# Kernel tuning notes

Hardware: AMD Instinct MI355X
Metric: run time of the kernel (lower is better)

## Reference

```python
import jax, jax.numpy as jnp
import numpy as np

N = 25000      # nodes
E = 400000     # edges
D = 128        # num_hidden (per-head out dim)
H = 3          # heads
NEG_SLOPE = 0.2
BN_EPS = 1e-5


def _gatv2(x, edge_index, Wl, bl, Wr, br, att, bias):
    """PyG GATv2Conv (concat=True, add_self_loops=True, dropout=0).
    x: [N, Din]; Wl/Wr: [Din, H*D]; att: [H, D]; bias: [H*D].
    """
    n = x.shape[0]
    h, d = att.shape
    loops = jnp.arange(n)
    src = jnp.concatenate([edge_index[0], loops])  # [E+N]
    dst = jnp.concatenate([edge_index[1], loops])
    xl = (x @ Wl + bl).reshape(n, h, d)  # source transform
    xr = (x @ Wr + br).reshape(n, h, d)  # target transform
    # edge scores: a^T LeakyReLU(xl_j + xr_i)
    e = jax.nn.leaky_relu(xl[src] + xr[dst], NEG_SLOPE)   # [E+N, H, D]
    score = jnp.einsum('ehd,hd->eh', e, att)              # [E+N, H]
    # segment softmax over incoming edges of each dst node
    m = jax.ops.segment_max(score, dst, num_segments=n)   # [N, H]
    ex = jnp.exp(score - m[dst])
    denom = jax.ops.segment_sum(ex, dst, num_segments=n)  # [N, H]
    alpha = ex / denom[dst]                               # [E+N, H]
    out = jax.ops.segment_sum(alpha[:, :, None] * xl[src], dst, num_segments=n)
    return out.reshape(n, h * d) + bias                   # [N, H*D]


def _batchnorm(x, gamma, beta):
    mu = jnp.mean(x, axis=0)
    var = jnp.var(x, axis=0)  # biased, as torch BN uses for normalization
    return gamma * (x - mu) * jax.lax.rsqrt(var + BN_EPS) + beta


def setup_inputs() -> dict:
    key = jax.random.key(0)
    ks = iter(jax.random.split(key, 32))
    s = 0.1
    p = {}
    p['x'] = jax.random.normal(next(ks), (N, D), jnp.float32)
    p['edge_index'] = jax.random.randint(next(ks), (2, E), 0, N, jnp.int64)
    for i in (1, 2):
        p[f'Wl{i}'] = s * jax.random.normal(next(ks), (D, H * D), jnp.float32)
        p[f'bl{i}'] = jnp.zeros((H * D,), jnp.float32)
        p[f'Wr{i}'] = s * jax.random.normal(next(ks), (D, H * D), jnp.float32)
        p[f'br{i}'] = jnp.zeros((H * D,), jnp.float32)
        p[f'att{i}'] = s * jax.random.normal(next(ks), (H, D), jnp.float32)
        p[f'bc{i}'] = jnp.zeros((H * D,), jnp.float32)
        p[f'g{i}'] = jnp.ones((D,), jnp.float32)
        p[f'be{i}'] = jnp.zeros((D,), jnp.float32)
    p['W1'] = s * jax.random.normal(next(ks), (H * D, D), jnp.float32)
    p['b1'] = jnp.zeros((D,), jnp.float32)
    p['W2'] = s * jax.random.normal(next(ks), (2 * H * D, D), jnp.float32)
    p['b2'] = jnp.zeros((D,), jnp.float32)
    return p


def reference(x, edge_index, Wl1, bl1, Wr1, br1, att1, bc1, g1, be1,
              Wl2, bl2, Wr2, br2, att2, bc2, g2, be2, W1, b1, W2, b2):
    x_in = _gatv2(x, edge_index, Wl1, bl1, Wr1, br1, att1, bc1)  # [N, H*D]
    h = _batchnorm(x_in @ W1 + b1, g1, be1)
    h = jax.nn.relu(h)                                           # [N, D]
    h2 = _gatv2(h, edge_index, Wl2, bl2, Wr2, br2, att2, bc2)    # [N, H*D]
    out = jnp.concatenate([h2, x_in], axis=1) @ W2 + b2          # [N, D]
    out = _batchnorm(out, g2, be2)
    return jax.nn.relu(out)
```

## Files before the change

### kernel.cpp

```cpp
#include <hip/hip_runtime.h>
#include <math.h>

#define NN 25000
#define NE 400000
#define DD 128
#define HD 384
#define NEG 0.2f
#define EPS 1e-5f

typedef unsigned int u32;
typedef unsigned short u16;
typedef __attribute__((ext_vector_type(8))) short short8;
typedef __attribute__((ext_vector_type(4))) float floatx4;

__device__ __forceinline__ u32 bf16_1(float x) {
    u32 u = __float_as_uint(x);
    return (u + 0x7fffu + ((u >> 16) & 1u)) >> 16;
}
__device__ __forceinline__ float blo(u32 u) { return __uint_as_float(u << 16); }
__device__ __forceinline__ float bhi(u32 u) { return __uint_as_float(u & 0xffff0000u); }

__device__ __forceinline__ void up8(uint4 u, float* f) {
    f[0] = blo(u.x); f[1] = bhi(u.x); f[2] = blo(u.y); f[3] = bhi(u.y);
    f[4] = blo(u.z); f[5] = bhi(u.z); f[6] = blo(u.w); f[7] = bhi(u.w);
}


__global__ void k_scan1(const int* __restrict__ cnt, int* __restrict__ bsum) {
    __shared__ int sh[256];
    int i = blockIdx.x * 256 + threadIdx.x;
    sh[threadIdx.x] = (i < NN) ? (cnt[i] + 1) : 0;
    __syncthreads();
    for (int o = 128; o >= 1; o >>= 1) {
        if ((int)threadIdx.x < o) sh[threadIdx.x] += sh[threadIdx.x + o];
        __syncthreads();
    }
    if (threadIdx.x == 0) bsum[blockIdx.x] = sh[0];
}

__global__ void k_scan3(const int* __restrict__ cnt, const int* __restrict__ bsum,
                        int* __restrict__ row_ptr, int* __restrict__ col_src,
                        int* __restrict__ cur) {
    __shared__ int sh[256];
    __shared__ int sb[128];
    int tid = threadIdx.x;
    if (tid < 128) sb[tid] = (tid < 98) ? bsum[tid] : 0;
    __syncthreads();
    for (int o = 1; o < 128; o <<= 1) {
        int t = (tid >= o && tid < 128) ? sb[tid - o] : 0;
        __syncthreads();
        if (tid < 128) sb[tid] += t;
        __syncthreads();
    }
    int i = blockIdx.x * 256 + tid;
    int v = (i < NN) ? (cnt[i] + 1) : 0;
    sh[tid] = v;
    __syncthreads();
    for (int o = 1; o < 256; o <<= 1) {
        int t = (tid >= o) ? sh[tid - o] : 0;
        __syncthreads();
        sh[tid] += t;
        __syncthreads();
    }
    int base = blockIdx.x ? sb[blockIdx.x - 1] : 0;
    if (i < NN) {
        int incl = base + sh[tid];
        row_ptr[i + 1] = incl;
        int p = incl - v;
        col_src[p] = i;
        cur[i] = p + 1;
    }
    if (i == 0) row_ptr[0] = 0;
}

__global__ void k_fill_edges(const int* __restrict__ src, const int* __restrict__ dst,
                             int* __restrict__ cur, int* __restrict__ col_src) {
    int e = blockIdx.x * 256 + threadIdx.x;
    if (e < NE) { int p = atomicAdd(&cur[dst[e]], 1); col_src[p] = src[e]; }
}

__global__ void k_cast_all(const float* __restrict__ x,
                           const float* __restrict__ Wl1, const float* __restrict__ Wr1,
                           const float* __restrict__ W1,
                           const float* __restrict__ Wl2, const float* __restrict__ Wr2,
                           const float* __restrict__ W2,
                           const float* __restrict__ bl1, const float* __restrict__ br1,
                           const float* __restrict__ bl2, const float* __restrict__ br2,
                           const int* __restrict__ edst,
                           u16* __restrict__ xb, u16* __restrict__ WfT1,
                           u16* __restrict__ W1T, u16* __restrict__ WfT2,
                           u16* __restrict__ W2T,
                           float* __restrict__ fb1, float* __restrict__ fb2,
                           int* __restrict__ cnt, float* __restrict__ stats) {
    int i = blockIdx.x * 256 + threadIdx.x;
    if (i < 400000) {
        const float4* xp = (const float4*)(x + (size_t)i * 8);
        float4 a = xp[0], b = xp[1];
        uint4 w;
        w.x = bf16_1(a.x) | (bf16_1(a.y) << 16);
        w.y = bf16_1(a.z) | (bf16_1(a.w) << 16);
        w.z = bf16_1(b.x) | (bf16_1(b.y) << 16);
        w.w = bf16_1(b.z) | (bf16_1(b.w) << 16);
        *(uint4*)(xb + (size_t)i * 8) = w;
        return;
    }
    i -= 400000;
    if (i < 400000) { atomicAdd(&cnt[edst[i]], 1); return; }
    i -= 400000;
    if (i < 49152) { int k = i / 384, n = i - k * 384; WfT1[n * 128 + k] = (u16)bf16_1(Wl1[i]); return; }
    i -= 49152;
    if (i < 49152) { int k = i / 384, n = i - k * 384; WfT1[(384 + n) * 128 + k] = (u16)bf16_1(Wr1[i]); return; }
    i -= 49152;
    if (i < 49152) { int k = i / 128, n = i - k * 128; W1T[n * 384 + k] = (u16)bf16_1(W1[i]); return; }
    i -= 49152;
    if (i < 49152) { int k = i / 384, n = i - k * 384; WfT2[n * 128 + k] = (u16)bf16_1(Wl2[i]); return; }
    i -= 49152;
    if (i < 49152) { int k = i / 384, n = i - k * 384; WfT2[(384 + n) * 128 + k] = (u16)bf16_1(Wr2[i]); return; }
    i -= 49152;
    if (i < 98304) { int k = i / 128, n = i - k * 128; W2T[n * 768 + k] = (u16)bf16_1(W2[i]); return; }
    i -= 98304;
    if (i < 768) { fb1[i] = (i < 384) ? bl1[i] : br1[i - 384]; return; }
    i -= 768;
    if (i < 768) { fb2[i] = (i < 384) ? bl2[i] : br2[i - 384]; return; }
    i -= 768;
    if (i < 512) stats[i] = 0.f;
}
#define CAST_TOTAL (400000 + 400000 + 5 * 49152 + 98304 + 1536 + 512)

__global__ __launch_bounds__(256) void k_gemm_k128(
        const u16* __restrict__ A, const u16* __restrict__ BT,
        const float* __restrict__ bias, u16* __restrict__ Cb, int M) {
    __shared__ short sA[128 * 128];
    __shared__ short sB[128 * 128];
    int tid = threadIdx.x;
    int wv = tid >> 6, lane = tid & 63;
    int quad = lane >> 4, m16 = lane & 15;
    int mb = blockIdx.y * 128, nb = blockIdx.x * 128;

#pragma unroll
    for (int j = 0; j < 8; ++j) {
        int L = j * 256 + tid;
        int r = L >> 4, c8 = (L & 15) ^ (r & 15);
        int gr = mb + r; gr = gr < M ? gr : M - 1;
        __builtin_amdgcn_global_load_lds(
            (const __attribute__((address_space(1))) void*)(A + (size_t)gr * 128 + c8 * 8),
            (__attribute__((address_space(3))) void*)(sA + (size_t)L * 8), 16, 0, 0);
    }
#pragma unroll
    for (int j = 0; j < 8; ++j) {
        int L = j * 256 + tid;
        int r = L >> 4, c8 = (L & 15) ^ (r & 15);
        __builtin_amdgcn_global_load_lds(
            (const __attribute__((address_space(1))) void*)(BT + (size_t)(nb + r) * 128 + c8 * 8),
            (__attribute__((address_space(3))) void*)(sB + (size_t)L * 8), 16, 0, 0);
    }
    __syncthreads();

    floatx4 acc[2][8];
#pragma unroll
    for (int mf = 0; mf < 2; ++mf)
#pragma unroll
        for (int nf = 0; nf < 8; ++nf)
#pragma unroll
            for (int r = 0; r < 4; ++r) acc[mf][nf][r] = 0.f;

#pragma unroll
    for (int ks = 0; ks < 4; ++ks) {
        int slot = (ks * 4 + quad) ^ m16;
        int row0 = wv * 32 + m16, row1 = row0 + 16;
        short8 a0 = *(const short8*)(sA + ((size_t)row0 * 16 + slot) * 8);
        short8 a1 = *(const short8*)(sA + ((size_t)row1 * 16 + slot) * 8);
#pragma unroll
        for (int nf = 0; nf < 8; ++nf) {
            short8 b = *(const short8*)(sB + ((size_t)(nf * 16 + m16) * 16 + slot) * 8);
            acc[0][nf] = __builtin_amdgcn_mfma_f32_16x16x32_bf16(a0, b, acc[0][nf], 0, 0, 0);
            acc[1][nf] = __builtin_amdgcn_mfma_f32_16x16x32_bf16(a1, b, acc[1][nf], 0, 0, 0);
        }
    }
    __syncthreads();

#pragma unroll
    for (int mf = 0; mf < 2; ++mf)
#pragma unroll
        for (int nf = 0; nf < 8; ++nf)
#pragma unroll
            for (int r = 0; r < 4; ++r) {
                int row = wv * 32 + mf * 16 + quad * 4 + r;
                int col = nf * 16 + m16;
                sA[row * 128 + col] = (short)bf16_1(acc[mf][nf][r] + bias[nb + col]);
            }
    __syncthreads();
    int xr = nb >= 384;
    int h = (xr ? (nb - 384) : nb) >> 7;
    u16* cb = Cb + ((size_t)(xr * 3 + h) * NN) * 128;
#pragma unroll
    for (int i = 0; i < 8; ++i) {
        int u = i * 256 + tid;
        int row = u >> 4, c8 = u & 15;
        int grow = mb + row;
        if (grow < M)
            *(uint4*)(cb + (size_t)grow * 128 + c8 * 8) = *(const uint4*)(sA + (size_t)u * 8);
    }
}

__global__ __launch_bounds__(256) void k_gemm_bf(
        const u16* __restrict__ A, const u16* __restrict__ BT,
        const float* __restrict__ bias,
        float* __restrict__ Cf, float* __restrict__ stats,
        int M, int N, int K, int lda) {
    __shared__ short smem[9216];
    short* sA = smem;
    short* sB = smem + 4096;
    int tid = threadIdx.x;
    int wv = tid >> 6, lane = tid & 63;
    int quad = lane >> 4, m16 = lane & 15;
    int sw = m16 & 7;
    int mb = blockIdx.y * 64, nb = blockIdx.x * 64;

    floatx4 acc[4];
#pragma unroll
    for (int nf = 0; nf < 4; ++nf)
#pragma unroll
        for (int r = 0; r < 4; ++r) acc[nf][r] = 0.f;

    for (int k0 = 0; k0 < K; k0 += 64) {
#pragma unroll
        for (int j = 0; j < 2; ++j) {
            int L = j * 256 + tid;
            int r = L >> 3, c8 = (L & 7) ^ (r & 7);
            int gr = mb + r; gr = gr < M ? gr : M - 1;
            __builtin_amdgcn_global_load_lds(
                (const __attribute__((address_space(1))) void*)(A + (size_t)gr * lda + k0 + c8 * 8),
                (__attribute__((address_space(3))) void*)(sA + (size_t)L * 8), 16, 0, 0);
        }
#pragma unroll
        for (int j = 0; j < 2; ++j) {
            int L = j * 256 + tid;
            int r = L >> 3, c8 = (L & 7) ^ (r & 7);
            __builtin_amdgcn_global_load_lds(
                (const __attribute__((address_space(1))) void*)(BT + (size_t)(nb + r) * K + k0 + c8 * 8),
                (__attribute__((address_space(3))) void*)(sB + (size_t)L * 8), 16, 0, 0);
        }
        __syncthreads();
#pragma unroll
        for (int ks = 0; ks < 2; ++ks) {
            int t = (ks * 4 + quad) ^ sw;
            const short* pa = sA + t * 8;
            const short* pb = sB + t * 8;
            short8 a0 = *(const short8*)(pa + (wv * 16 + m16) * 64);
#pragma unroll
            for (int nf = 0; nf < 4; ++nf) {
                short8 b = *(const short8*)(pb + (nf * 16 + m16) * 64);
                acc[nf] = __builtin_amdgcn_mfma_f32_16x16x32_bf16(a0, b, acc[nf], 0, 0, 0);
            }
        }
        __syncthreads();
    }
    float* fs = (float*)smem;
#pragma unroll
    for (int nf = 0; nf < 4; ++nf)
#pragma unroll
        for (int r = 0; r < 4; ++r) {
            int row = wv * 16 + quad * 4 + r;
            int col = nf * 16 + m16;
            fs[row * 64 + col] = acc[nf][r] + (bias ? bias[nb + col] : 0.f);
        }
    __syncthreads();
#pragma unroll
    for (int i = 0; i < 4; ++i) {
        int u = i * 256 + tid;
        int row = u >> 4, c4 = u & 15;
        int grow = mb + row;
        if (grow < M)
            *(float4*)(Cf + (size_t)grow * N + nb + c4 * 4) = *(const float4*)(fs + (size_t)u * 4);
    }
    if (stats) {
        float* ps = (float*)(smem + 8192);
        int col = tid & 63, qr = tid >> 6;
        int vr = M - mb; vr = vr < 64 ? vr : 64;
        int r0 = qr * 16, r1 = r0 + 16 < vr ? r0 + 16 : vr;
        float s = 0.f, q = 0.f;
        for (int r = r0; r < r1; ++r) { float v = fs[r * 64 + col]; s += v; q += v * v; }
        ps[qr * 64 + col] = s;
        ps[256 + qr * 64 + col] = q;
        __syncthreads();
        if (tid < 64) {
            float ss = ps[tid] + ps[64 + tid] + ps[128 + tid] + ps[192 + tid];
            atomicAdd(&stats[nb + tid], ss);
        } else if (tid < 128) {
            int c = tid - 64;
            float qq = ps[256 + c] + ps[320 + c] + ps[384 + c] + ps[448 + c];
            atomicAdd(&stats[128 + nb + c], qq);
        }
    }
}

__global__ __launch_bounds__(256) void k_gat_h(const u32* __restrict__ XLb,
                                               const u32* __restrict__ XRb,
                                               const float* __restrict__ att,
                                               const float* __restrict__ bias,
                                               const int* __restrict__ row_ptr,
                                               const int* __restrict__ col_src,
                                               u32* __restrict__ outb) {
    int h = blockIdx.y;
    const u32* XLh = XLb + (size_t)h * NN * 64;
    const u32* XRh = XRb + (size_t)h * NN * 64;
    int node = blockIdx.x * 4 + (threadIdx.x >> 6);
    int lane = threadIdx.x & 63;
    int g = lane >> 4, gl = lane & 15;

    float xr_f[8], att_f[8], acc[8];
    up8(*(const uint4*)(XRh + (size_t)node * 64 + 4 * gl), xr_f);
    *(float4*)&att_f[0] = *(const float4*)&att[h * 128 + 8 * gl];
    *(float4*)&att_f[4] = *(const float4*)&att[h * 128 + 8 * gl + 4];
#pragma unroll
    for (int k = 0; k < 8; ++k) acc[k] = 0.f;
    float l = 0.f;

    int e0 = row_ptr[node];
    int cntE = row_ptr[node + 1] - e0;
    int elast = e0 + cntE - 1;

    int ea = e0 + g;     ea = ea < elast ? ea : elast;
    int eb = e0 + g + 4; eb = eb < elast ? eb : elast;
    uint4 ua = *(const uint4*)(XLh + (size_t)col_src[ea] * 64 + 4 * gl);
    uint4 ub = *(const uint4*)(XLh + (size_t)col_src[eb] * 64 + 4 * gl);

    for (int t = g; t < cntE; t += 8) {
        int e2 = e0 + t + 8;  e2 = e2 < elast ? e2 : elast;
        int e3 = e0 + t + 12; e3 = e3 < elast ? e3 : elast;
        uint4 un0 = *(const uint4*)(XLh + (size_t)col_src[e2] * 64 + 4 * gl);
        uint4 un1 = *(const uint4*)(XLh + (size_t)col_src[e3] * 64 + 4 * gl);

        float xa[8], xb[8];
        up8(ua, xa); up8(ub, xb);
        float pa = 0.f, pb = 0.f;
#pragma unroll
        for (int k = 0; k < 8; ++k) {
            float va = xa[k] + xr_f[k];
            float vb = xb[k] + xr_f[k];
            pa = fmaf(fmaxf(va, NEG * va), att_f[k], pa);
            pb = fmaf(fmaxf(vb, NEG * vb), att_f[k], pb);
        }
#pragma unroll
        for (int o = 1; o <= 8; o <<= 1) {
            pa += __shfl_xor(pa, o);
            pb += __shfl_xor(pb, o);
        }
        float wa = __expf(pa);
        float wb = ((t + 4) < cntE) ? __expf(pb) : 0.f;
        l += wa + wb;
#pragma unroll
        for (int k = 0; k < 8; ++k)
            acc[k] = fmaf(wa, xa[k], fmaf(wb, xb[k], acc[k]));

        ua = un0; ub = un1;
    }

#pragma unroll
    for (int o = 16; o <= 32; o <<= 1) {
        l += __shfl_xor(l, o);
#pragma unroll
        for (int k = 0; k < 8; ++k) acc[k] += __shfl_xor(acc[k], o);
    }

    if (g == 0) {
        float r = 1.f / l;
        float bv[8];
        *(float4*)&bv[0] = *(const float4*)&bias[h * 128 + 8 * gl];
        *(float4*)&bv[4] = *(const float4*)&bias[h * 128 + 8 * gl + 4];
        uint4 w;
        w.x = bf16_1(fmaf(acc[0], r, bv[0])) | (bf16_1(fmaf(acc[1], r, bv[1])) << 16);
        w.y = bf16_1(fmaf(acc[2], r, bv[2])) | (bf16_1(fmaf(acc[3], r, bv[3])) << 16);
        w.z = bf16_1(fmaf(acc[4], r, bv[4])) | (bf16_1(fmaf(acc[5], r, bv[5])) << 16);
        w.w = bf16_1(fmaf(acc[6], r, bv[6])) | (bf16_1(fmaf(acc[7], r, bv[7])) << 16);
        *(uint4*)(outb + (size_t)node * 384 + h * 64 + 4 * gl) = w;
    }
}

__global__ void k_bn_apply(float* __restrict__ y, const float* __restrict__ stats,
                           const float* __restrict__ g, const float* __restrict__ be,
                           u16* __restrict__ yb, int wf) {
    int i = blockIdx.x * 256 + threadIdx.x;
    if (i >= NN * DD / 8) return;
    int idx = i * 8;
    int c0 = idx & 127;
    float v[8];
    *(float4*)&v[0] = *(const float4*)(y + idx);
    *(float4*)&v[4] = *(const float4*)(y + idx + 4);
    const float minv = 1.f / (float)NN;
#pragma unroll
    for (int k = 0; k < 8; ++k) {
        int c = c0 + k;
        float mu = stats[c] * minv;
        float var = stats[128 + c] * minv - mu * mu;
        float sc = g[c] * rsqrtf(var + EPS);
        float sh = be[c] - mu * sc;
        v[k] = fmaxf(fmaf(v[k], sc, sh), 0.f);
    }
    if (wf) {
        *(float4*)(y + idx) = *(const float4*)&v[0];
        *(float4*)(y + idx + 4) = *(const float4*)&v[4];
    }
    if (yb) {
        uint4 w;
        w.x = bf16_1(v[0]) | (bf16_1(v[1]) << 16);
        w.y = bf16_1(v[2]) | (bf16_1(v[3]) << 16);
        w.z = bf16_1(v[4]) | (bf16_1(v[5]) << 16);
        w.w = bf16_1(v[6]) | (bf16_1(v[7]) << 16);
        *(uint4*)(yb + idx) = w;
    }
}


extern "C" void kernel_launch(void* const* d_in, const int* in_sizes, int n_in,
                              void* d_out, int out_size, void* d_ws, size_t ws_size,
                              hipStream_t stream) {
    const float* x    = (const float*)d_in[0];
    const int*   ei   = (const int*)d_in[1];
    const float* Wl1  = (const float*)d_in[2];
    const float* bl1  = (const float*)d_in[3];
    const float* Wr1  = (const float*)d_in[4];
    const float* br1  = (const float*)d_in[5];
    const float* att1 = (const float*)d_in[6];
    const float* bc1  = (const float*)d_in[7];
    const float* g1   = (const float*)d_in[8];
    const float* be1  = (const float*)d_in[9];
    const float* Wl2  = (const float*)d_in[10];
    const float* bl2  = (const float*)d_in[11];
    const float* Wr2  = (const float*)d_in[12];
    const float* br2  = (const float*)d_in[13];
    const float* att2 = (const float*)d_in[14];
    const float* bc2  = (const float*)d_in[15];
    const float* g2   = (const float*)d_in[16];
    const float* be2  = (const float*)d_in[17];
    const float* W1   = (const float*)d_in[18];
    const float* b1   = (const float*)d_in[19];
    const float* W2   = (const float*)d_in[20];
    const float* b2   = (const float*)d_in[21];
    const int* esrc = ei;
    const int* edst = ei + NE;
    float* out = (float*)d_out;

    float* bufD   = (float*)d_ws;
    float* stats  = bufD + 3200000;
    int* row_ptr  = (int*)(stats + 512);
    int* cnt      = row_ptr + 25002;
    int* col_src  = cnt + 25000;
    int* bsum     = col_src + 425000;
    float* fb1    = (float*)(bsum + 132);
    float* fb2    = fb1 + 768;
    u16* xb       = (u16*)(fb2 + 768);
    u16* XLb      = xb + 3200000;
    u16* XRb      = XLb + 3 * NN * 128;
    u16* bufCat   = XRb + 3 * NN * 128;
    u16* bufDb    = bufCat + 19200000;
    u16* WfT1     = bufDb + 3200000;
    u16* W1T      = WfT1 + 98304;
    u16* WfT2     = W1T + 49152;
    u16* W2T      = WfT2 + 98304;

    hipMemsetAsync(cnt, 0, NN * sizeof(int), stream);
    k_cast_all<<<(CAST_TOTAL + 255) / 256, 256, 0, stream>>>(
        x, Wl1, Wr1, W1, Wl2, Wr2, W2, bl1, br1, bl2, br2, edst,
        xb, WfT1, W1T, WfT2, W2T, fb1, fb2, cnt, stats);

    k_scan1<<<98, 256, 0, stream>>>(cnt, bsum);
    k_scan3<<<98, 256, 0, stream>>>(cnt, bsum, row_ptr, col_src, cnt);
    k_fill_edges<<<(NE + 255) / 256, 256, 0, stream>>>(esrc, edst, cnt, col_src);

    dim3 blk(256);
    dim3 gK(6, (NN + 127) / 128);
    dim3 g64(2, (NN + 63) / 64);
    dim3 gGat((NN + 3) / 4, 3);

    k_gemm_k128<<<gK, blk, 0, stream>>>(xb, WfT1, fb1, XLb, NN);
    k_gat_h<<<gGat, blk, 0, stream>>>((const u32*)XLb, (const u32*)XRb, att1, bc1,
                                      row_ptr, col_src, (u32*)bufCat + 192);

    k_gemm_bf<<<g64, blk, 0, stream>>>(bufCat + 384, W1T, b1, bufD, stats, NN, DD, HD, 768);
    k_bn_apply<<<(NN * DD / 8 + 255) / 256, 256, 0, stream>>>(bufD, stats, g1, be1, bufDb, 0);

    k_gemm_k128<<<gK, blk, 0, stream>>>(bufDb, WfT2, fb2, XLb, NN);
    k_gat_h<<<gGat, blk, 0, stream>>>((const u32*)XLb, (const u32*)XRb, att2, bc2,
                                      row_ptr, col_src, (u32*)bufCat);

    k_gemm_bf<<<g64, blk, 0, stream>>>(bufCat, W2T, b2, out, stats + 256, NN, DD, 768, 768);
    k_bn_apply<<<(NN * DD / 8 + 255) / 256, 256, 0, stream>>>(out, stats + 256, g2, be2, nullptr, 1);
}
```

Baseline: 384.8 us.

## Fuse three GAT heads into one kernel with packed-f32 math and exp2 scaling

Replaces the per-head GAT aggregation grid (one launch dimension per head) with a single kernel where each wave handles all three heads of a node, so the col_src index loads and row_ptr reads are shared across heads. Leaky ReLU is rewritten as 0.6*v + 0.4*|v| (with the 0.6 factored into the pre-scaled attention vector) and evaluated with packed v_pk_add/v_pk_fma f32 instructions. The attention vector is pre-multiplied by 0.6*log2(e) so exp2 can be used in place of exp. Edge prefetch drops from two edges per group to one edge across three heads. Register pressure rises from the three-head accumulators, which may lower occupancy.

```diff
diff --git a/kernel.cpp b/kernel.cpp
--- a/kernel.cpp
+++ b/kernel.cpp
@@ -12,6 +12,7 @@
 typedef unsigned short u16;
 typedef __attribute__((ext_vector_type(8))) short short8;
 typedef __attribute__((ext_vector_type(4))) float floatx4;
+typedef __attribute__((ext_vector_type(2))) float f32x2;
 
 __device__ __forceinline__ u32 bf16_1(float x) {
     u32 u = __float_as_uint(x);
@@ -23,6 +24,24 @@
 __device__ __forceinline__ void up8(uint4 u, float* f) {
     f[0] = blo(u.x); f[1] = bhi(u.x); f[2] = blo(u.y); f[3] = bhi(u.y);
     f[4] = blo(u.z); f[5] = bhi(u.z); f[6] = blo(u.w); f[7] = bhi(u.w);
+}
+__device__ __forceinline__ void up8f2(uint4 u, f32x2* f) {
+    f[0] = f32x2{blo(u.x), bhi(u.x)};
+    f[1] = f32x2{blo(u.y), bhi(u.y)};
+    f[2] = f32x2{blo(u.z), bhi(u.z)};
+    f[3] = f32x2{blo(u.w), bhi(u.w)};
+}
+
+__device__ __forceinline__ f32x2 pk_add(f32x2 a, f32x2 b) {
+    f32x2 d; asm("v_pk_add_f32 %0, %1, %2" : "=v"(d) : "v"(a), "v"(b)); return d;
+}
+__device__ __forceinline__ f32x2 pk_fma(f32x2 a, f32x2 b, f32x2 c) {
+    f32x2 d; asm("v_pk_fma_f32 %0, %1, %2, %3" : "=v"(d) : "v"(a), "v"(b), "v"(c)); return d;
+}
+__device__ __forceinline__ f32x2 fabs2(f32x2 v) {
+    u32 a = __float_as_uint(v.x) & 0x7fffffffu;
+    u32 b = __float_as_uint(v.y) & 0x7fffffffu;
+    return f32x2{__uint_as_float(a), __uint_as_float(b)};
 }
 
 
@@ -86,11 +105,13 @@
                            const float* __restrict__ W2,
                            const float* __restrict__ bl1, const float* __restrict__ br1,
                            const float* __restrict__ bl2, const float* __restrict__ br2,
+                           const float* __restrict__ att1, const float* __restrict__ att2,
                            const int* __restrict__ edst,
                            u16* __restrict__ xb, u16* __restrict__ WfT1,
                            u16* __restrict__ W1T, u16* __restrict__ WfT2,
                            u16* __restrict__ W2T,
                            float* __restrict__ fb1, float* __restrict__ fb2,
+                           float* __restrict__ attc1, float* __restrict__ attc2,
                            int* __restrict__ cnt, float* __restrict__ stats) {
     int i = blockIdx.x * 256 + threadIdx.x;
     if (i < 400000) {
@@ -123,9 +144,13 @@
     i -= 768;
     if (i < 768) { fb2[i] = (i < 384) ? bl2[i] : br2[i - 384]; return; }
     i -= 768;
+    if (i < 384) { attc1[i] = att1[i] * 0.86561702f; return; }
+    i -= 384;
+    if (i < 384) { attc2[i] = att2[i] * 0.86561702f; return; }
+    i -= 384;
     if (i < 512) stats[i] = 0.f;
 }
-#define CAST_TOTAL (400000 + 400000 + 5 * 49152 + 98304 + 1536 + 512)
+#define CAST_TOTAL (400000 + 400000 + 5 * 49152 + 98304 + 1536 + 768 + 512)
 
 __global__ __launch_bounds__(256) void k_gemm_k128(
         const u16* __restrict__ A, const u16* __restrict__ BT,
@@ -295,86 +320,104 @@
     }
 }
 
-__global__ __launch_bounds__(256) void k_gat_h(const u32* __restrict__ XLb,
-                                               const u32* __restrict__ XRb,
-                                               const float* __restrict__ att,
-                                               const float* __restrict__ bias,
-                                               const int* __restrict__ row_ptr,
-                                               const int* __restrict__ col_src,
-                                               u32* __restrict__ outb) {
-    int h = blockIdx.y;
-    const u32* XLh = XLb + (size_t)h * NN * 64;
-    const u32* XRh = XRb + (size_t)h * NN * 64;
+__global__ __launch_bounds__(256) void k_gat3(
+        const u32* __restrict__ XLb, const u32* __restrict__ XRb,
+        const float* __restrict__ attc, const float* __restrict__ bias,
+        const int* __restrict__ row_ptr, const int* __restrict__ col_src,
+        u32* __restrict__ outb) {
     int node = blockIdx.x * 4 + (threadIdx.x >> 6);
     int lane = threadIdx.x & 63;
     int g = lane >> 4, gl = lane & 15;
 
-    float xr_f[8], att_f[8], acc[8];
-    up8(*(const uint4*)(XRh + (size_t)node * 64 + 4 * gl), xr_f);
-    *(float4*)&att_f[0] = *(const float4*)&att[h * 128 + 8 * gl];
-    *(float4*)&att_f[4] = *(const float4*)&att[h * 128 + 8 * gl + 4];
-#pragma unroll
-    for (int k = 0; k < 8; ++k) acc[k] = 0.f;
-    float l = 0.f;
+    const u32* XL0 = XLb;
+    const u32* XL1 = XLb + (size_t)NN * 64;
+    const u32* XL2 = XLb + (size_t)2 * NN * 64;
+
+    f32x2 xr[3][4], a6[3][4], acc[3][4];
+    float l[3];
+    const f32x2 c23 = {0.66666667f, 0.66666667f};
+#pragma unroll
+    for (int h = 0; h < 3; ++h) {
+        uint4 u = *(const uint4*)(XRb + (size_t)h * NN * 64 + (size_t)node * 64 + 4 * gl);
+        up8f2(u, xr[h]);
+#pragma unroll
+        for (int j = 0; j < 4; ++j) {
+            a6[h][j] = *(const f32x2*)(attc + h * 128 + 8 * gl + 2 * j);
+            acc[h][j] = f32x2{0.f, 0.f};
+        }
+        l[h] = 0.f;
+    }
 
     int e0 = row_ptr[node];
-    int cntE = row_ptr[node + 1] - e0;
-    int elast = e0 + cntE - 1;
-
-    int ea = e0 + g;     ea = ea < elast ? ea : elast;
-    int eb = e0 + g + 4; eb = eb < elast ? eb : elast;
-    uint4 ua = *(const uint4*)(XLh + (size_t)col_src[ea] * 64 + 4 * gl);
-    uint4 ub = *(const uint4*)(XLh + (size_t)col_src[eb] * 64 + 4 * gl);
-
-    for (int t = g; t < cntE; t += 8) {
-        int e2 = e0 + t + 8;  e2 = e2 < elast ? e2 : elast;
-        int e3 = e0 + t + 12; e3 = e3 < elast ? e3 : elast;
-        uint4 un0 = *(const uint4*)(XLh + (size_t)col_src[e2] * 64 + 4 * gl);
-        uint4 un1 = *(const uint4*)(XLh + (size_t)col_src[e3] * 64 + 4 * gl);
-
-        float xa[8], xb[8];
-        up8(ua, xa); up8(ub, xb);
-        float pa = 0.f, pb = 0.f;
-#pragma unroll
-        for (int k = 0; k < 8; ++k) {
-            float va = xa[k] + xr_f[k];
-            float vb = xb[k] + xr_f[k];
-            pa = fmaf(fmaxf(va, NEG * va), att_f[k], pa);
-            pb = fmaf(fmaxf(vb, NEG * vb), att_f[k], pb);
-        }
-#pragma unroll
-        for (int o = 1; o <= 8; o <<= 1) {
-            pa += __shfl_xor(pa, o);
-            pb += __shfl_xor(pb, o);
-        }
-        float wa = __expf(pa);
-        float wb = ((t + 4) < cntE) ? __expf(pb) : 0.f;
-        l += wa + wb;
-#pragma unroll
-        for (int k = 0; k < 8; ++k)
-            acc[k] = fmaf(wa, xa[k], fmaf(wb, xb[k], acc[k]));
-
-        ua = un0; ub = un1;
+    int cnt = row_ptr[node + 1] - e0;
+    int elast = e0 + cnt - 1;
+
+    int ea = e0 + g; ea = ea < elast ? ea : elast;
+    u32 voff = (u32)col_src[ea] * 64 + 4 * gl;
+    uint4 u0 = *(const uint4*)(XL0 + voff);
+    uint4 u1 = *(const uint4*)(XL1 + voff);
+    uint4 u2 = *(const uint4*)(XL2 + voff);
+
+    for (int t = g; t < cnt; t += 4) {
+        int en = e0 + t + 4; en = en < elast ? en : elast;
+        u32 voffn = (u32)col_src[en] * 64 + 4 * gl;
+        uint4 n0 = *(const uint4*)(XL0 + voffn);
+        uint4 n1 = *(const uint4*)(XL1 + voffn);
+        uint4 n2 = *(const uint4*)(XL2 + voffn);
+
+#pragma unroll
+        for (int h = 0; h < 3; ++h) {
+            uint4 uh = (h == 0) ? u0 : (h == 1) ? u1 : u2;
+            f32x2 xa[4];
+            up8f2(uh, xa);
+            f32x2 p2 = {0.f, 0.f};
+#pragma unroll
+            for (int j = 0; j < 4; ++j) {
+                f32x2 v = pk_add(xa[j], xr[h][j]);
+                f32x2 tt = pk_fma(fabs2(v), c23, v);
+                p2 = pk_fma(tt, a6[h][j], p2);
+            }
+            float p = p2.x + p2.y;
+#pragma unroll
+            for (int o = 1; o <= 8; o <<= 1) p += __shfl_xor(p, o);
+            float w = __builtin_amdgcn_exp2f(p);
+            l[h] += w;
+            f32x2 w2 = {w, w};
+#pragma unroll
+            for (int j = 0; j < 4; ++j) acc[h][j] = pk_fma(xa[j], w2, acc[h][j]);
+        }
+        u0 = n0; u1 = n1; u2 = n2;
     }
 
 #pragma unroll
     for (int o = 16; o <= 32; o <<= 1) {
-        l += __shfl_xor(l, o);
-#pragma unroll
-        for (int k = 0; k < 8; ++k) acc[k] += __shfl_xor(acc[k], o);
+#pragma unroll
+        for (int h = 0; h < 3; ++h) {
+            l[h] += __shfl_xor(l[h], o);
+#pragma unroll
+            for (int j = 0; j < 4; ++j) {
+                f32x2 s;
+                s.x = __shfl_xor(acc[h][j].x, o);
+                s.y = __shfl_xor(acc[h][j].y, o);
+                acc[h][j] = pk_add(acc[h][j], s);
+            }
+        }
     }
 
     if (g == 0) {
-        float r = 1.f / l;
-        float bv[8];
-        *(float4*)&bv[0] = *(const float4*)&bias[h * 128 + 8 * gl];
-        *(float4*)&bv[4] = *(const float4*)&bias[h * 128 + 8 * gl + 4];
-        uint4 w;
-        w.x = bf16_1(fmaf(acc[0], r, bv[0])) | (bf16_1(fmaf(acc[1], r, bv[1])) << 16);
-        w.y = bf16_1(fmaf(acc[2], r, bv[2])) | (bf16_1(fmaf(acc[3], r, bv[3])) << 16);
-        w.z = bf16_1(fmaf(acc[4], r, bv[4])) | (bf16_1(fmaf(acc[5], r, bv[5])) << 16);
-        w.w = bf16_1(fmaf(acc[6], r, bv[6])) | (bf16_1(fmaf(acc[7], r, bv[7])) << 16);
-        *(uint4*)(outb + (size_t)node * 384 + h * 64 + 4 * gl) = w;
+#pragma unroll
+        for (int h = 0; h < 3; ++h) {
+            float r = 1.f / l[h];
+            float bv[8];
+            *(float4*)&bv[0] = *(const float4*)&bias[h * 128 + 8 * gl];
+            *(float4*)&bv[4] = *(const float4*)&bias[h * 128 + 8 * gl + 4];
+            uint4 w;
+            w.x = bf16_1(fmaf(acc[h][0].x, r, bv[0])) | (bf16_1(fmaf(acc[h][0].y, r, bv[1])) << 16);
+            w.y = bf16_1(fmaf(acc[h][1].x, r, bv[2])) | (bf16_1(fmaf(acc[h][1].y, r, bv[3])) << 16);
+            w.z = bf16_1(fmaf(acc[h][2].x, r, bv[4])) | (bf16_1(fmaf(acc[h][2].y, r, bv[5])) << 16);
+            w.w = bf16_1(fmaf(acc[h][3].x, r, bv[6])) | (bf16_1(fmaf(acc[h][3].y, r, bv[7])) << 16);
+            *(uint4*)(outb + (size_t)node * 384 + h * 64 + 4 * gl) = w;
+        }
     }
 }
 
@@ -450,7 +493,9 @@
     int* bsum     = col_src + 425000;
     float* fb1    = (float*)(bsum + 132);
     float* fb2    = fb1 + 768;
-    u16* xb       = (u16*)(fb2 + 768);
+    float* attc1  = fb2 + 768;
+    float* attc2  = attc1 + 384;
+    u16* xb       = (u16*)(attc2 + 384);
     u16* XLb      = xb + 3200000;
     u16* XRb      = XLb + 3 * NN * 128;
     u16* bufCat   = XRb + 3 * NN * 128;
@@ -462,8 +507,8 @@
 
     hipMemsetAsync(cnt, 0, NN * sizeof(int), stream);
     k_cast_all<<<(CAST_TOTAL + 255) / 256, 256, 0, stream>>>(
-        x, Wl1, Wr1, W1, Wl2, Wr2, W2, bl1, br1, bl2, br2, edst,
-        xb, WfT1, W1T, WfT2, W2T, fb1, fb2, cnt, stats);
+        x, Wl1, Wr1, W1, Wl2, Wr2, W2, bl1, br1, bl2, br2, att1, att2, edst,
+        xb, WfT1, W1T, WfT2, W2T, fb1, fb2, attc1, attc2, cnt, stats);
 
     k_scan1<<<98, 256, 0, stream>>>(cnt, bsum);
     k_scan3<<<98, 256, 0, stream>>>(cnt, bsum, row_ptr, col_src, cnt);
@@ -472,18 +517,18 @@
     dim3 blk(256);
     dim3 gK(6, (NN + 127) / 128);
     dim3 g64(2, (NN + 63) / 64);
-    dim3 gGat((NN + 3) / 4, 3);
+    dim3 gGat((NN + 3) / 4);
 
     k_gemm_k128<<<gK, blk, 0, stream>>>(xb, WfT1, fb1, XLb, NN);
-    k_gat_h<<<gGat, blk, 0, stream>>>((const u32*)XLb, (const u32*)XRb, att1, bc1,
-                                      row_ptr, col_src, (u32*)bufCat + 192);
+    k_gat3<<<gGat, blk, 0, stream>>>((const u32*)XLb, (const u32*)XRb, attc1, bc1,
+                                     row_ptr, col_src, (u32*)bufCat + 192);
 
     k_gemm_bf<<<g64, blk, 0, stream>>>(bufCat + 384, W1T, b1, bufD, stats, NN, DD, HD, 768);
     k_bn_apply<<<(NN * DD / 8 + 255) / 256, 256, 0, stream>>>(bufD, stats, g1, be1, bufDb, 0);
 
     k_gemm_k128<<<gK, blk, 0, stream>>>(bufDb, WfT2, fb2, XLb, NN);
-    k_gat_h<<<gGat, blk, 0, stream>>>((const u32*)XLb, (const u32*)XRb, att2, bc2,
-                                      row_ptr, col_src, (u32*)bufCat);
+    k_gat3<<<gGat, blk, 0, stream>>>((const u32*)XLb, (const u32*)XRb, attc2, bc2,
+                                     row_ptr, col_src, (u32*)bufCat);
 
     k_gemm_bf<<<g64, blk, 0, stream>>>(bufCat, W2T, b2, out, stats + 256, NN, DD, 768, 768);
     k_bn_apply<<<(NN * DD / 8 + 255) / 256, 256, 0, stream>>>(out, stats + 256, g2, be2, nullptr, 1);
```

Result: slower. 416.5 us (+8.2%).
